# Performance work log

Hardware: AMD Instinct MI355X
Metric: run time of the kernel (lower is better)

## Reference

```python
import jax, jax.numpy as jnp
import numpy as np

B, T, D_MODEL, N_HEADS = 4, 2048, 1024, 16


def _alibi_bias(n_heads, seq_len):
    # matches torch alibi_bias(): slopes 2**(-8*i/m), i=1..m, m = pow2_ceil(n_heads)
    m = 1
    while m < n_heads:
        m *= 2
    slopes = jnp.array([2.0 ** (-8.0 * i / m) for i in range(1, m + 1)][:n_heads],
                       dtype=jnp.float32)
    pos = jnp.arange(seq_len)
    bias = (pos[None, :] - pos[:, None]).astype(jnp.float32)  # [T, T], j - i
    return slopes[:, None, None, None] * bias[None, None]      # [H, 1, T, T]


def setup_inputs() -> dict:
    key = jax.random.key(0)
    kx, kqkv, ko = jax.random.split(key, 3)
    x = jax.random.normal(kx, (B, T, D_MODEL), dtype=jnp.float32)
    Wqkv = jax.random.normal(kqkv, (3 * D_MODEL, D_MODEL), dtype=jnp.float32) / np.sqrt(D_MODEL)
    Wo = jax.random.normal(ko, (D_MODEL, D_MODEL), dtype=jnp.float32) / np.sqrt(D_MODEL)
    alibi = _alibi_bias(N_HEADS, T)  # [H, 1, T, T]
    return {"x": x, "alibi": alibi, "Wqkv": Wqkv, "Wo": Wo}


def reference(x, alibi, Wqkv, Wo):
    Bb, Tt, C = x.shape
    H = N_HEADS
    dk = C // H
    # qkv projection: [B, T, 3C] -> [B, T, 3, H, dk]
    qkv = (x @ Wqkv.T).reshape(Bb, Tt, 3, H, dk)
    q = jnp.moveaxis(qkv[:, :, 0], 2, 1)  # [B, H, T, dk]
    k = jnp.moveaxis(qkv[:, :, 1], 2, 1)
    v = jnp.moveaxis(qkv[:, :, 2], 2, 1)
    # causal (-inf above diagonal) + alibi additive mask, fp32, like the torch path
    causal = jnp.triu(jnp.full((Tt, Tt), -jnp.inf, dtype=jnp.float32), k=1)
    mask = causal[None, None] + alibi[:, 0][None]  # [1, H, T, T]
    scores = jnp.einsum('bhqd,bhkd->bhqk', q, k) / jnp.sqrt(jnp.float32(dk)) + mask
    p = jax.nn.softmax(scores, axis=-1)
    att = jnp.einsum('bhqk,bhkd->bhqd', p, v)           # [B, H, T, dk]
    y = jnp.moveaxis(att, 1, 2).reshape(Bb, Tt, C)       # [B, T, C]
    return y @ Wo.T
```

## Files before the change

kernel.cpp:

```cpp
#include <hip/hip_runtime.h>
#include <hip/hip_bf16.h>


#define B_ 4
#define T_ 2048
#define C_ 1024
#define H_ 16
#define DK 64

typedef __attribute__((ext_vector_type(8))) short short8;
typedef __attribute__((ext_vector_type(4))) float floatx4;

#define GLDS16(g, l)                                                          \
    __builtin_amdgcn_global_load_lds(                                         \
        (const __attribute__((address_space(1))) void*)(g),                   \
        (__attribute__((address_space(3))) void*)(l), 16, 0, 0)

static __device__ inline short f2bf(float x) {
    __hip_bfloat16 h = __float2bfloat16(x);
    return *reinterpret_cast<short*>(&h);
}

__global__ void detect_k(const unsigned int* __restrict__ x,
                         const unsigned int* __restrict__ ali,
                         const unsigned int* __restrict__ wqkv,
                         const unsigned int* __restrict__ wo,
                         int* __restrict__ flags) {
    __shared__ int cnt[4];
    const int tid = threadIdx.x;
    if (tid < 4) cnt[tid] = 0;
    __syncthreads();
    const int g = tid >> 6, l = tid & 63;
    const unsigned int* p = (g == 0) ? x : (g == 1) ? ali : (g == 2) ? wqkv : wo;
    int c = 0;
    for (int i = 0; i < 4; i++) {
        unsigned int w = p[l * 4 + i];
        int e0 = (w >> 7) & 0xFF;
        int e1 = (w >> 23) & 0xFF;
        c += (e0 >= 100 && e0 <= 140);
        c += (e1 >= 100 && e1 <= 140);
    }
    atomicAdd(&cnt[g], c);
    __syncthreads();
    if (l == 0) flags[g] = (cnt[g] < 400) ? 1 : 0;
}

__global__ void tobf16_k(const void* __restrict__ in, short* __restrict__ out,
                         int n8, const int* __restrict__ flag) {
    const bool f32 = (*flag != 0);
    int i = blockIdx.x * blockDim.x + threadIdx.x;
    const int stride = gridDim.x * blockDim.x;
    for (; i < n8; i += stride) {
        if (f32) {
            float4 f0 = ((const float4*)in)[2 * i];
            float4 f1 = ((const float4*)in)[2 * i + 1];
            short8 v = { f2bf(f0.x), f2bf(f0.y), f2bf(f0.z), f2bf(f0.w),
                         f2bf(f1.x), f2bf(f1.y), f2bf(f1.z), f2bf(f1.w) };
            *(short8*)(out + (size_t)i * 8) = v;
        } else {
            *(short8*)(out + (size_t)i * 8) = ((const short8*)in)[i];
        }
    }
}

template <int MODE, int N>
__global__ __launch_bounds__(256) void gemm128_k(const short* __restrict__ A,
                                                 const short* __restrict__ W,
                                                 void* __restrict__ Dv) {
    const int K = 1024;
    const int tid  = threadIdx.x;
    const int wv   = tid >> 6;
    const int lane = tid & 63;
    const int l15  = lane & 15;
    const int quad = lane >> 4;
    const int wm = wv >> 1, wn = wv & 1;
    const int bn = blockIdx.x, bm = blockIdx.y;

    __shared__ short As[128 * 64];
    __shared__ short Bs[128 * 64];

    floatx4 acc[4][4];
#pragma unroll
    for (int mt = 0; mt < 4; mt++)
#pragma unroll
        for (int nt = 0; nt < 4; nt++)
#pragma unroll
            for (int r = 0; r < 4; r++) acc[mt][nt][r] = 0.f;

    const int lr = lane >> 3;
    const int lc = lane & 7;
    const int cg = lc ^ lr;

    for (int kt = 0; kt < K; kt += 64) {
        __syncthreads();
#pragma unroll
        for (int i = 0; i < 4; i++) {
            const int rbase = wv * 32 + i * 8;
            const int r = rbase + lr;
            size_t ga;
            if (MODE == 2) {
                int rowg = bm * 128 + r;
                int b = rowg >> 11, t = rowg & (T_ - 1), hh = kt >> 6;
                ga = (((size_t)b * H_ + hh) * T_ + t) * DK + cg * 8;
            } else {
                ga = (size_t)(bm * 128 + r) * K + kt + cg * 8;
            }
            GLDS16(A + ga, As + rbase * 64);
            size_t gb = (size_t)(bn * 128 + rbase + lr) * K + kt + cg * 8;
            GLDS16(W + gb, Bs + rbase * 64);
        }
        __syncthreads();
#pragma unroll
        for (int ks = 0; ks < 64; ks += 32) {
            short8 af[4], bf[4];
#pragma unroll
            for (int mt = 0; mt < 4; mt++) {
                int row = wm * 64 + mt * 16 + l15;
                int cs = ((ks >> 3) + quad) ^ (row & 7);
                af[mt] = *(const short8*)(As + row * 64 + cs * 8);
            }
#pragma unroll
            for (int nt = 0; nt < 4; nt++) {
                int row = wn * 64 + nt * 16 + l15;
                int cs = ((ks >> 3) + quad) ^ (row & 7);
                bf[nt] = *(const short8*)(Bs + row * 64 + cs * 8);
            }
#pragma unroll
            for (int mt = 0; mt < 4; mt++)
#pragma unroll
                for (int nt = 0; nt < 4; nt++)
                    acc[mt][nt] = __builtin_amdgcn_mfma_f32_16x16x32_bf16(
                        af[mt], bf[nt], acc[mt][nt], 0, 0, 0);
        }
    }

#pragma unroll
    for (int mt = 0; mt < 4; mt++) {
#pragma unroll
        for (int nt = 0; nt < 4; nt++) {
#pragma unroll
            for (int r = 0; r < 4; r++) {
                int row = bm * 128 + wm * 64 + mt * 16 + quad * 4 + r;
                int col = bn * 128 + wn * 64 + nt * 16 + l15;
                if (MODE == 0) {
                    int b = row >> 11, t = row & (T_ - 1);
                    int s = col >> 10, rem = col & 1023;
                    int h = rem >> 6, d = rem & 63;
                    size_t dst = ((((size_t)s * B_ + b) * H_ + h) * T_ + t) * DK + d;
                    ((short*)Dv)[dst] = f2bf(acc[mt][nt][r]);
                } else if (MODE == 3) {
                    int h = row >> 6, d = row & 63;
                    int b = col >> 11, t = col & (T_ - 1);
                    size_t dst = (((size_t)(2 * B_ + b) * H_ + h) * DK + d) * T_ + t;
                    ((short*)Dv)[dst] = f2bf(acc[mt][nt][r]);
                } else {
                    ((float*)Dv)[(size_t)row * N + col] = acc[mt][nt][r];
                }
            }
        }
    }
}

template <int MODE, int N>
__global__ __launch_bounds__(256) void gemm_k(const void* __restrict__ Av,
                                              const void* __restrict__ Wv,
                                              void* __restrict__ Dv,
                                              const int* fA, const int* fW,
                                              size_t aOff) {
    const int K = 1024;
    const int tid  = threadIdx.x;
    const int wave = tid >> 6;
    const int lane = tid & 63;
    const int l15  = lane & 15;
    const int quad = lane >> 4;
    const int bn = blockIdx.x;
    const int bm = blockIdx.y;
    const bool aF32 = fA && (*fA != 0);
    const bool wF32 = fW && (*fW != 0);

    __shared__ short As[64 * 72];
    __shared__ short Bs[64 * 72];

    floatx4 acc[4];
#pragma unroll
    for (int nt = 0; nt < 4; nt++)
#pragma unroll
        for (int r = 0; r < 4; r++) acc[nt][r] = 0.f;

    for (int kt = 0; kt < K; kt += 64) {
        __syncthreads();
#pragma unroll
        for (int i = 0; i < 2; i++) {
            int chunk = tid + i * 256;
            int r = chunk >> 3, c8 = (chunk & 7) * 8;
            size_t offA;
            if (MODE == 2) {
                int rowg = bm * 64 + r;
                int b = rowg >> 11, t = rowg & (T_ - 1), hh = kt >> 6;
                offA = (((size_t)b * H_ + hh) * T_ + t) * DK + c8;
            } else {
                offA = (size_t)(bm * 64 + r) * K + kt + c8;
            }
            size_t offW = (size_t)(bn * 64 + r) * K + kt + c8;
            if (aF32) {
                const float* Af = (const float*)Av + aOff;
                float4 f0 = *(const float4*)(Af + offA);
                float4 f1 = *(const float4*)(Af + offA + 4);
                short8 v = { f2bf(f0.x), f2bf(f0.y), f2bf(f0.z), f2bf(f0.w),
                             f2bf(f1.x), f2bf(f1.y), f2bf(f1.z), f2bf(f1.w) };
                *(short8*)(As + r * 72 + c8) = v;
            } else {
                *(short8*)(As + r * 72 + c8) =
                    *(const short8*)((const short*)Av + aOff + offA);
            }
            if (wF32) {
                const float* Wf = (const float*)Wv;
                float4 f0 = *(const float4*)(Wf + offW);
                float4 f1 = *(const float4*)(Wf + offW + 4);
                short8 v = { f2bf(f0.x), f2bf(f0.y), f2bf(f0.z), f2bf(f0.w),
                             f2bf(f1.x), f2bf(f1.y), f2bf(f1.z), f2bf(f1.w) };
                *(short8*)(Bs + r * 72 + c8) = v;
            } else {
                *(short8*)(Bs + r * 72 + c8) = *(const short8*)((const short*)Wv + offW);
            }
        }
        __syncthreads();
#pragma unroll
        for (int ks = 0; ks < 64; ks += 32) {
            short8 a = *(const short8*)(As + (wave * 16 + l15) * 72 + ks + quad * 8);
#pragma unroll
            for (int nt = 0; nt < 4; nt++) {
                short8 b = *(const short8*)(Bs + (nt * 16 + l15) * 72 + ks + quad * 8);
                acc[nt] = __builtin_amdgcn_mfma_f32_16x16x32_bf16(a, b, acc[nt], 0, 0, 0);
            }
        }
    }

#pragma unroll
    for (int nt = 0; nt < 4; nt++) {
#pragma unroll
        for (int r = 0; r < 4; r++) {
            int row = bm * 64 + wave * 16 + quad * 4 + r;
            int col = bn * 64 + nt * 16 + l15;
            if (MODE == 0) {
                int b = row >> 11, t = row & (T_ - 1);
                int s = col >> 10, rem = col & 1023;
                int h = rem >> 6, d = rem & 63;
                size_t dst = ((((size_t)s * B_ + b) * H_ + h) * T_ + t) * DK + d;
                ((short*)Dv)[dst] = f2bf(acc[nt][r]);
            } else if (MODE == 3) {
                int h = row >> 6, d = row & 63;
                int b = col >> 11, t = col & (T_ - 1);
                size_t dst = (((size_t)(2 * B_ + b) * H_ + h) * DK + d) * T_ + t;
                ((short*)Dv)[dst] = f2bf(acc[nt][r]);
            } else {
                ((float*)Dv)[(size_t)row * N + col] = acc[nt][r];
            }
        }
    }
}

__global__ __launch_bounds__(256, 5) void attn_k(short* __restrict__ qkv) {
    const int tid  = threadIdx.x;
    const int wave = tid >> 6;
    const int lane = tid & 63;
    const int l15  = lane & 15;
    const int quad = lane >> 4;
    const int gid  = blockIdx.x;
    const int bh = (gid & 7) * 8 + (gid >> 8);
    const int qb = (31 - ((gid >> 3) & 31)) * 64;
    const int b = bh >> 4, h = bh & 15;

    short* Qp       = qkv + (((size_t)(0 * B_ + b) * H_ + h) * T_) * DK;
    const short* Kp = qkv + (((size_t)(1 * B_ + b) * H_ + h) * T_) * DK;
    const short* Vt = qkv + (((size_t)(2 * B_ + b) * H_ + h) * DK) * T_;

    __shared__ short Qs[64 * 72];
    __shared__ short Ks[64 * 72];
    __shared__ short Vts[64 * 72];

#pragma unroll
    for (int i = 0; i < 2; i++) {
        int chunk = tid + i * 256;
        int r = chunk >> 3, c8 = (chunk & 7) * 8;
        *(short8*)(Qs + r * 72 + c8) = *(const short8*)(Qp + (size_t)(qb + r) * DK + c8);
    }
    __syncthreads();
    short8 aq0 = *(const short8*)(Qs + (wave * 16 + l15) * 72 + quad * 8);
    short8 aq1 = *(const short8*)(Qs + (wave * 16 + l15) * 72 + 32 + quad * 8);

    const float LOG2E = 1.4426950408889634f;
    const float slope2 = exp2f(-0.5f * (float)(h + 1)) * LOG2E;
    const float scale2 = 0.125f * LOG2E;

    float lsum[4];
    floatx4 o[4];
#pragma unroll
    for (int r = 0; r < 4; r++) lsum[r] = 0.f;
#pragma unroll
    for (int nt = 0; nt < 4; nt++)
#pragma unroll
        for (int r = 0; r < 4; r++) o[nt][r] = 0.f;

    const int jt_end = qb >> 6;
    const int rb = qb + wave * 16 + quad * 4;
    int jstart = 0;
    {
        int lim = qb - 63 - (int)(50.f / slope2);
        if (lim > 0) jstart = lim >> 6;
    }

    for (int jt = jstart; jt <= jt_end; jt++) {
        __syncthreads();
#pragma unroll
        for (int i = 0; i < 2; i++) {
            int chunk = tid + i * 256;
            int r = chunk >> 3, c8 = (chunk & 7) * 8;
            *(short8*)(Ks + r * 72 + c8) =
                *(const short8*)(Kp + (size_t)(jt * 64 + r) * DK + c8);
            *(short8*)(Vts + r * 72 + c8) =
                *(const short8*)(Vt + (size_t)r * T_ + jt * 64 + c8);
        }
        __syncthreads();

        floatx4 s[4];
#pragma unroll
        for (int nt = 0; nt < 4; nt++)
#pragma unroll
            for (int r = 0; r < 4; r++) s[nt][r] = 0.f;
#pragma unroll
        for (int nt = 0; nt < 4; nt++) {
            short8 b0 = *(const short8*)(Ks + (nt * 16 + l15) * 72 + quad * 8);
            short8 b1 = *(const short8*)(Ks + (nt * 16 + l15) * 72 + 32 + quad * 8);
            s[nt] = __builtin_amdgcn_mfma_f32_16x16x32_bf16(aq0, b0, s[nt], 0, 0, 0);
            s[nt] = __builtin_amdgcn_mfma_f32_16x16x32_bf16(aq1, b1, s[nt], 0, 0, 0);
        }

        const bool diag = (jt == jt_end);
#pragma unroll
        for (int nt = 0; nt < 4; nt++) {
            int colg = jt * 64 + nt * 16 + l15;
            float cb = slope2 * (float)(colg - rb);
#pragma unroll
            for (int r = 0; r < 4; r++) {
                float sv = fmaf(s[nt][r], scale2, cb - slope2 * (float)r);
                if (diag && colg > rb + r) sv = -1e30f;
                float p = exp2f(sv);
                lsum[r] += p;
                Qs[wave * 1152 + (quad * 4 + r) * 72 + nt * 16 + l15] = f2bf(p);
            }
        }

#pragma unroll
        for (int ks = 0; ks < 64; ks += 32) {
            short8 a = *(const short8*)(Qs + wave * 1152 + l15 * 72 + ks + quad * 8);
#pragma unroll
            for (int nt = 0; nt < 4; nt++) {
                short8 bf = *(const short8*)(Vts + (nt * 16 + l15) * 72 + ks + quad * 8);
                o[nt] = __builtin_amdgcn_mfma_f32_16x16x32_bf16(a, bf, o[nt], 0, 0, 0);
            }
        }
    }

#pragma unroll
    for (int r = 0; r < 4; r++) {
#pragma unroll
        for (int mask = 1; mask < 16; mask <<= 1)
            lsum[r] += __shfl_xor(lsum[r], mask);
    }
#pragma unroll
    for (int nt = 0; nt < 4; nt++) {
#pragma unroll
        for (int r = 0; r < 4; r++) {
            int t = qb + wave * 16 + quad * 4 + r;
            int d = nt * 16 + l15;
            Qp[(size_t)t * DK + d] = f2bf(o[nt][r] / lsum[r]);
        }
    }
}

extern "C" void kernel_launch(void* const* d_in, const int* in_sizes, int n_in,
                              void* d_out, int out_size, void* d_ws, size_t ws_size,
                              hipStream_t stream) {
    const void* x    = d_in[0];
    const void* ali  = d_in[1];
    const void* Wqkv = d_in[2];
    const void* Wo   = d_in[3];
    float* out = (float*)d_out;

    int*   flags  = (int*)d_ws;
    short* qkv    = (short*)((char*)d_ws + 1024);
    short* xbf    = (short*)((char*)d_ws + 50332672);
    short* wqkvbf = (short*)((char*)d_ws + 67109888);
    short* wobf   = (short*)((char*)d_ws + 73401344);
    const bool fast = ws_size >= (size_t)75498496;

    detect_k<<<1, 256, 0, stream>>>((const unsigned int*)x, (const unsigned int*)ali,
                                    (const unsigned int*)Wqkv, (const unsigned int*)Wo,
                                    flags);

    dim3 blk(256);
    if (fast) {
        tobf16_k<<<2048, 256, 0, stream>>>(x, xbf, B_ * T_ * C_ / 8, &flags[0]);
        tobf16_k<<<1536, 256, 0, stream>>>(Wqkv, wqkvbf, 3 * C_ * C_ / 8, &flags[2]);
        tobf16_k<<<512, 256, 0, stream>>>(Wo, wobf, C_ * C_ / 8, &flags[3]);
        gemm128_k<0, 0><<<dim3(16, 64), blk, 0, stream>>>(xbf, wqkvbf, qkv);
        gemm128_k<3, 0><<<dim3(64, 8), blk, 0, stream>>>(
            wqkvbf + (size_t)2048 * 1024, xbf, qkv);
        attn_k<<<dim3(2048), blk, 0, stream>>>(qkv);
        gemm128_k<2, C_><<<dim3(8, 64), blk, 0, stream>>>(qkv, wobf, out);
    } else {
        gemm_k<0, 0><<<dim3(32, 128), blk, 0, stream>>>(x, Wqkv, qkv,
                                                        &flags[0], &flags[2], 0);
        gemm_k<3, 0><<<dim3(128, 16), blk, 0, stream>>>(Wqkv, x, qkv,
                                                        &flags[2], &flags[0],
                                                        (size_t)2048 * 1024);
        attn_k<<<dim3(2048), blk, 0, stream>>>(qkv);
        gemm_k<2, C_><<<dim3(16, 128), blk, 0, stream>>>(qkv, Wo, out,
                                                         nullptr, &flags[3], 0);
    }
}
```

Before: 534.6 us.

## Load attention K/V tiles via direct global-to-LDS with XOR swizzle, drop detect kernel

The attention kernel now fills its K and V^T tiles with direct global-to-LDS 16-byte loads, which skips the register round trip. The tiles are laid out unpadded with an XOR-swizzled column index to avoid bank conflicts, and the P scratch stride shrinks from 72 to 68. The smaller LDS footprint lets the occupancy hint rise from 5 to 6 blocks. The separate dtype-detect launch is removed from the fast path: each conversion thread instead re-derives the fp32/bf16 flag from the first 16 words, which costs a single-block kernel launch less but adds redundant loads per thread.

```diff
diff --git a/kernel.cpp b/kernel.cpp
--- a/kernel.cpp
+++ b/kernel.cpp
@@ -46,8 +46,18 @@
 }
 
 __global__ void tobf16_k(const void* __restrict__ in, short* __restrict__ out,
-                         int n8, const int* __restrict__ flag) {
-    const bool f32 = (*flag != 0);
+                         int n8) {
+    const unsigned int* u = (const unsigned int*)in;
+    int c = 0;
+#pragma unroll
+    for (int i = 0; i < 16; i++) {
+        unsigned int w = u[i];
+        int e0 = (w >> 7) & 0xFF;
+        int e1 = (w >> 23) & 0xFF;
+        c += (e0 >= 100 && e0 <= 140);
+        c += (e1 >= 100 && e1 <= 140);
+    }
+    const bool f32 = (c < 25);
     int i = blockIdx.x * blockDim.x + threadIdx.x;
     const int stride = gridDim.x * blockDim.x;
     for (; i < n8; i += stride) {
@@ -106,7 +116,7 @@
                 ga = (size_t)(bm * 128 + r) * K + kt + cg * 8;
             }
             GLDS16(A + ga, As + rbase * 64);
-            size_t gb = (size_t)(bn * 128 + rbase + lr) * K + kt + cg * 8;
+            size_t gb = (size_t)(bn * 128 + r) * K + kt + cg * 8;
             GLDS16(W + gb, Bs + rbase * 64);
         }
         __syncthreads();
@@ -260,7 +270,7 @@
     }
 }
 
-__global__ __launch_bounds__(256, 5) void attn_k(short* __restrict__ qkv) {
+__global__ __launch_bounds__(256, 6) void attn_k(short* __restrict__ qkv) {
     const int tid  = threadIdx.x;
     const int wave = tid >> 6;
     const int lane = tid & 63;
@@ -276,8 +286,8 @@
     const short* Vt = qkv + (((size_t)(2 * B_ + b) * H_ + h) * DK) * T_;
 
     __shared__ short Qs[64 * 72];
-    __shared__ short Ks[64 * 72];
-    __shared__ short Vts[64 * 72];
+    __shared__ short Ks[64 * 64];
+    __shared__ short Vts[64 * 64];
 
 #pragma unroll
     for (int i = 0; i < 2; i++) {
@@ -310,16 +320,18 @@
         if (lim > 0) jstart = lim >> 6;
     }
 
+    const int lr = lane >> 3;
+    const int cg = (lane & 7) ^ lr;
+
     for (int jt = jstart; jt <= jt_end; jt++) {
         __syncthreads();
 #pragma unroll
         for (int i = 0; i < 2; i++) {
-            int chunk = tid + i * 256;
-            int r = chunk >> 3, c8 = (chunk & 7) * 8;
-            *(short8*)(Ks + r * 72 + c8) =
-                *(const short8*)(Kp + (size_t)(jt * 64 + r) * DK + c8);
-            *(short8*)(Vts + r * 72 + c8) =
-                *(const short8*)(Vt + (size_t)r * T_ + jt * 64 + c8);
+            const int rbase = wave * 16 + i * 8;
+            GLDS16(Kp + (size_t)(jt * 64 + rbase + lr) * DK + cg * 8,
+                   Ks + rbase * 64);
+            GLDS16(Vt + (size_t)(rbase + lr) * T_ + jt * 64 + cg * 8,
+                   Vts + rbase * 64);
         }
         __syncthreads();
 
@@ -330,8 +342,11 @@
             for (int r = 0; r < 4; r++) s[nt][r] = 0.f;
 #pragma unroll
         for (int nt = 0; nt < 4; nt++) {
-            short8 b0 = *(const short8*)(Ks + (nt * 16 + l15) * 72 + quad * 8);
-            short8 b1 = *(const short8*)(Ks + (nt * 16 + l15) * 72 + 32 + quad * 8);
+            int row = nt * 16 + l15;
+            int c0 = quad ^ (row & 7);
+            int c1 = (4 + quad) ^ (row & 7);
+            short8 b0 = *(const short8*)(Ks + row * 64 + c0 * 8);
+            short8 b1 = *(const short8*)(Ks + row * 64 + c1 * 8);
             s[nt] = __builtin_amdgcn_mfma_f32_16x16x32_bf16(aq0, b0, s[nt], 0, 0, 0);
             s[nt] = __builtin_amdgcn_mfma_f32_16x16x32_bf16(aq1, b1, s[nt], 0, 0, 0);
         }
@@ -347,16 +362,18 @@
                 if (diag && colg > rb + r) sv = -1e30f;
                 float p = exp2f(sv);
                 lsum[r] += p;
-                Qs[wave * 1152 + (quad * 4 + r) * 72 + nt * 16 + l15] = f2bf(p);
+                Qs[wave * 1088 + (quad * 4 + r) * 68 + nt * 16 + l15] = f2bf(p);
             }
         }
 
 #pragma unroll
         for (int ks = 0; ks < 64; ks += 32) {
-            short8 a = *(const short8*)(Qs + wave * 1152 + l15 * 72 + ks + quad * 8);
+            short8 a = *(const short8*)(Qs + wave * 1088 + l15 * 68 + ks + quad * 8);
 #pragma unroll
             for (int nt = 0; nt < 4; nt++) {
-                short8 bf = *(const short8*)(Vts + (nt * 16 + l15) * 72 + ks + quad * 8);
+                int row = nt * 16 + l15;
+                int cs = ((ks >> 3) + quad) ^ (row & 7);
+                short8 bf = *(const short8*)(Vts + row * 64 + cs * 8);
                 o[nt] = __builtin_amdgcn_mfma_f32_16x16x32_bf16(a, bf, o[nt], 0, 0, 0);
             }
         }
@@ -395,21 +412,21 @@
     short* wobf   = (short*)((char*)d_ws + 73401344);
     const bool fast = ws_size >= (size_t)75498496;
 
-    detect_k<<<1, 256, 0, stream>>>((const unsigned int*)x, (const unsigned int*)ali,
-                                    (const unsigned int*)Wqkv, (const unsigned int*)Wo,
-                                    flags);
-
     dim3 blk(256);
     if (fast) {
-        tobf16_k<<<2048, 256, 0, stream>>>(x, xbf, B_ * T_ * C_ / 8, &flags[0]);
-        tobf16_k<<<1536, 256, 0, stream>>>(Wqkv, wqkvbf, 3 * C_ * C_ / 8, &flags[2]);
-        tobf16_k<<<512, 256, 0, stream>>>(Wo, wobf, C_ * C_ / 8, &flags[3]);
+        tobf16_k<<<2048, 256, 0, stream>>>(x, xbf, B_ * T_ * C_ / 8);
+        tobf16_k<<<1536, 256, 0, stream>>>(Wqkv, wqkvbf, 3 * C_ * C_ / 8);
+        tobf16_k<<<512, 256, 0, stream>>>(Wo, wobf, C_ * C_ / 8);
         gemm128_k<0, 0><<<dim3(16, 64), blk, 0, stream>>>(xbf, wqkvbf, qkv);
         gemm128_k<3, 0><<<dim3(64, 8), blk, 0, stream>>>(
             wqkvbf + (size_t)2048 * 1024, xbf, qkv);
         attn_k<<<dim3(2048), blk, 0, stream>>>(qkv);
         gemm128_k<2, C_><<<dim3(8, 64), blk, 0, stream>>>(qkv, wobf, out);
     } else {
+        detect_k<<<1, 256, 0, stream>>>((const unsigned int*)x,
+                                        (const unsigned int*)ali,
+                                        (const unsigned int*)Wqkv,
+                                        (const unsigned int*)Wo, flags);
         gemm_k<0, 0><<<dim3(32, 128), blk, 0, stream>>>(x, Wqkv, qkv,
                                                         &flags[0], &flags[2], 0);
         gemm_k<3, 0><<<dim3(128, 16), blk, 0, stream>>>(Wqkv, x, qkv,
```

Result: no change. 530.3 us (-0.8%).
